# Optimization experiments

Measured on AMD Instinct MI355X. Metric: run time of the kernel, lower is better.

Reference implementation:

```python
import jax, jax.numpy as jnp
import numpy as np

N, E, C = 50000, 600000, 128
BN_EPS = 1e-5
NORM_EPS = 1e-12


def _edgeconv(x, src, dst, wa, ba, g, be, rm, rv, wb, bb):
    # PyG EdgeConv: message = MLP(concat(x_i, x_j - x_i)); aggr='add' at target i
    x_i = x[dst]                      # [E, C] target features
    x_j = x[src]                      # [E, C] source features
    m = jnp.concatenate([x_i, x_j - x_i], axis=-1)   # [E, 2C]
    m = jax.nn.relu(m @ wa.T + ba)                   # Linear(2C->C) + ReLU
    m = (m - rm) * (g * jax.lax.rsqrt(rv + BN_EPS)) + be  # BatchNorm1d (eval)
    m = m @ wb.T + bb                                # Linear(C->C)
    return jax.ops.segment_sum(m, dst, num_segments=x.shape[0])  # [N, C]


def _lin(k, fan_in, shape):
    bound = 1.0 / np.sqrt(fan_in)
    return jax.random.uniform(k, shape, jnp.float32, -bound, bound)


def setup_inputs() -> dict:
    key = jax.random.key(0)
    ks = jax.random.split(key, 16)
    inp = {
        "x": jax.random.normal(ks[0], (N, C), jnp.float32),
        "edge_index": jax.random.randint(ks[1], (2, E), 0, N, jnp.int64),
    }
    # layer 1 params
    inp["w1a"] = _lin(ks[2], 2 * C, (C, 2 * C)); inp["b1a"] = _lin(ks[3], 2 * C, (C,))
    inp["g1"] = jnp.ones((C,), jnp.float32) + 0.1 * jax.random.normal(ks[4], (C,))
    inp["be1"] = 0.1 * jax.random.normal(ks[5], (C,))
    inp["rm1"] = 0.1 * jax.random.normal(ks[6], (C,))
    inp["rv1"] = 0.5 + jax.random.uniform(ks[7], (C,))
    inp["w1b"] = _lin(ks[8], C, (C, C)); inp["b1b"] = _lin(ks[9], C, (C,))
    # layer 2 params
    inp["w2a"] = _lin(ks[10], 2 * C, (C, 2 * C)); inp["b2a"] = _lin(ks[11], 2 * C, (C,))
    inp["g2"] = jnp.ones((C,), jnp.float32) + 0.1 * jax.random.normal(ks[12], (C,))
    inp["be2"] = 0.1 * jax.random.normal(ks[13], (C,))
    inp["rm2"] = 0.1 * jax.random.normal(ks[14], (C,))
    inp["rv2"] = 0.5 + jax.random.uniform(ks[15], (C,))
    k2 = jax.random.split(ks[15], 2)
    inp["w2b"] = _lin(k2[0], C, (C, C)); inp["b2b"] = _lin(k2[1], C, (C,))
    return inp


def reference(x, edge_index, w1a, b1a, g1, be1, rm1, rv1, w1b, b1b,
              w2a, b2a, g2, be2, rm2, rv2, w2b, b2b):
    src, dst = edge_index[0], edge_index[1]
    # layer 1 (all but last): conv -> relu -> L2 normalize -> dropout(eval=identity)
    h = _edgeconv(x, src, dst, w1a, b1a, g1, be1, rm1, rv1, w1b, b1b)
    h = jax.nn.relu(h)
    h = h / jnp.maximum(jnp.linalg.norm(h, axis=-1, keepdims=True), NORM_EPS)
    # last layer: conv only
    return _edgeconv(h, src, dst, w2a, b2a, g2, be2, rm2, rv2, w2b, b2b)
```

## Files before the change

kernel.cpp:

```cpp
#include <hip/hip_runtime.h>

#define CCH 128
#define WPAD 136
typedef unsigned short ushort;
typedef __attribute__((ext_vector_type(8))) short bf16x8_t;
typedef __attribute__((ext_vector_type(4))) float f32x4;

union ABu { bf16x8_t v; ushort u[8]; uint4 q; };

__device__ __forceinline__ ushort f2b(float f) {
  union { float f; unsigned u; } v{f};
  unsigned r = v.u + 0x7fffu + ((v.u >> 16) & 1u);
  return (ushort)(r >> 16);
}
__device__ __forceinline__ float b2f(ushort s) {
  union { unsigned u; float f; } v{(unsigned)s << 16};
  return v.f;
}

__global__ __launch_bounds__(256) void k_pre(const float* __restrict__ w1a,
                                             const float* __restrict__ w1b,
                                             const float* __restrict__ w2a,
                                             const float* __restrict__ w2b,
                                             ushort* __restrict__ Wcat1, ushort* __restrict__ Wb1,
                                             ushort* __restrict__ Wcat2, ushort* __restrict__ Wb2,
                                             const void* __restrict__ ei, int* __restrict__ deg,
                                             int E) {
  const int b = blockIdx.x, t = threadIdx.x;
  if (b < 128) {
    int i = b * 256 + t;
    int c = i >> 7, k = i & 127;
    float v = (c < 128) ? w1a[c * 256 + k] - w1a[c * 256 + 128 + k]
                        : w1a[(c - 128) * 256 + 128 + k];
    Wcat1[i] = f2b(v);
    if (i < 16384) Wb1[i] = f2b(w1b[i]);
  } else if (b < 256) {
    int i = (b - 128) * 256 + t;
    int c = i >> 7, k = i & 127;
    float v = (c < 128) ? w2a[c * 256 + k] - w2a[c * 256 + 128 + k]
                        : w2a[(c - 128) * 256 + 128 + k];
    Wcat2[i] = f2b(v);
    if (i < 16384) Wb2[i] = f2b(w2b[i]);
  } else {
    __shared__ int nz;
    if (t == 0) nz = 0;
    __syncthreads();
    int e = (b - 256) * 256 + t;
    unsigned hi = (e < E) ? ((const unsigned*)ei)[2 * (size_t)e + 1] : 0u;
    if (hi) atomicAdd(&nz, 1);
    __syncthreads();
    bool i64 = (nz == 0);
    if (e < E) {
      int d = i64 ? (int)((const long long*)ei)[(size_t)E + e]
                  : ((const int*)ei)[(size_t)E + e];
      atomicAdd(&deg[d], 1);
    }
  }
}

__global__ __launch_bounds__(256) void k_rowptr(const int* __restrict__ deg,
                                                const int* __restrict__ bsum,
                                                int* __restrict__ rowptr,
                                                int n, int nb, int Etot) {
  __shared__ int s[256];
  const int t = threadIdx.x, b = blockIdx.x;
  s[t] = (t < nb && t < b) ? bsum[t] : 0;
  __syncthreads();
  for (int off = 128; off > 0; off >>= 1) {
    if (t < off) s[t] += s[t + off];
    __syncthreads();
  }
  int boffset = s[0];
  __syncthreads();
  int i = b * 256 + t;
  int v = (i < n) ? deg[i] : 0;
  s[t] = v; __syncthreads();
  for (int off = 1; off < 256; off <<= 1) {
    int tv = (t >= off) ? s[t - off] : 0;
    __syncthreads();
    s[t] += tv;
    __syncthreads();
  }
  if (i < n) rowptr[i] = boffset + s[t] - v;
  if (b == gridDim.x - 1 && t == 0) rowptr[n] = Etot;
}

__global__ __launch_bounds__(256) void k_scatter(const void* __restrict__ ei,
                                                 const int* __restrict__ rowptr,
                                                 int* __restrict__ cnt,
                                                 int* __restrict__ esrc, int E) {
  __shared__ int nz;
  const int t = threadIdx.x;
  if (t == 0) nz = 0;
  __syncthreads();
  int e = blockIdx.x * 256 + t;
  unsigned hi = (e < E) ? ((const unsigned*)ei)[2 * (size_t)e + 1] : 0u;
  if (hi) atomicAdd(&nz, 1);
  __syncthreads();
  bool i64 = (nz == 0);
  if (e < E) {
    int d, sv;
    if (i64) {
      sv = (int)((const long long*)ei)[(size_t)e];
      d  = (int)((const long long*)ei)[(size_t)E + e];
    } else {
      sv = ((const int*)ei)[(size_t)e];
      d  = ((const int*)ei)[(size_t)E + e];
    }
    int pos = rowptr[d] + atomicAdd(&cnt[d], 1);
    esrc[pos] = sv;
  }
}

__device__ __forceinline__ void stage_w(const ushort* __restrict__ Wp,
                                        ushort* __restrict__ wlds, int t) {
  for (int i = t; i < 128 * 16; i += 256) {
    int row = i >> 4, ch = i & 15;
    *(uint4*)&wlds[row * WPAD + ch * 8] = *(const uint4*)&Wp[row * CCH + ch * 8];
  }
}

__device__ __forceinline__ void load_a1_bf16(const ushort* __restrict__ XB,
                                             int ar, int quad, int nN, ABu a[4]) {
#pragma unroll
  for (int kk = 0; kk < 4; ++kk)
    a[kk].q = (ar < nN) ? *(const uint4*)(XB + (size_t)ar * CCH + kk * 32 + quad * 8)
                        : make_uint4(0, 0, 0, 0);
}

__device__ __forceinline__ void load_a1_f32(const float* __restrict__ X,
                                            int ar, int quad, int nN, ABu a[4]) {
#pragma unroll
  for (int kk = 0; kk < 4; ++kk) {
    if (ar < nN) {
      const float* p = X + (size_t)ar * CCH + kk * 32 + quad * 8;
      float4 f0 = *(const float4*)p, f1 = *(const float4*)(p + 4);
      a[kk].u[0] = f2b(f0.x); a[kk].u[1] = f2b(f0.y);
      a[kk].u[2] = f2b(f0.z); a[kk].u[3] = f2b(f0.w);
      a[kk].u[4] = f2b(f1.x); a[kk].u[5] = f2b(f1.y);
      a[kk].u[6] = f2b(f1.z); a[kk].u[7] = f2b(f1.w);
    } else a[kk].q = make_uint4(0, 0, 0, 0);
  }
}

__device__ __forceinline__ void load_a1_lds(const ushort* __restrict__ hlds,
                                            int lr, int quad, ABu a[4]) {
#pragma unroll
  for (int kk = 0; kk < 4; ++kk)
    a[kk].q = *(const uint4*)&hlds[lr * WPAD + kk * 32 + quad * 8];
}

__device__ __forceinline__ void mma1(const ABu a[4],
                                     const ushort* __restrict__ wlds,
                                     int ln, int quad, f32x4 acc[8]) {
#pragma unroll
  for (int s = 0; s < 8; ++s) acc[s] = (f32x4){0.f, 0.f, 0.f, 0.f};
#pragma unroll
  for (int s = 0; s < 8; ++s) {
#pragma unroll
    for (int kk = 0; kk < 4; ++kk) {
      ABu b;
      b.q = *(const uint4*)&wlds[(s * 16 + ln) * WPAD + kk * 32 + quad * 8];
      acc[s] = __builtin_amdgcn_mfma_f32_16x16x32_bf16(a[kk].v, b.v, acc[s], 0, 0, 0);
    }
  }
}

__device__ __forceinline__ void epi1(f32x4 acc[8], int rowb, int ln, int quad, int nN,
                                     const float* bias, int half, ushort* dst) {
#pragma unroll
  for (int s = 0; s < 8; ++s) {
    int col = s * 16 + ln;
    float bv = half ? 0.f : bias[col];
#pragma unroll
    for (int r = 0; r < 4; ++r) {
      int row = rowb + quad * 4 + r;
      if (row < nN) dst[(size_t)row * CCH + col] = f2b(acc[s][r] + bv);
    }
  }
}

__global__ __launch_bounds__(256) void k_mix1(const float* __restrict__ x,
                                              const ushort* __restrict__ Wcat,
                                              const float* __restrict__ bias,
                                              ushort* __restrict__ A1,
                                              ushort* __restrict__ A2, int nN,
                                              const int* __restrict__ deg,
                                              int* __restrict__ bsum, int gG, int n) {
  __shared__ ushort wlds[128 * WPAD];
  const int t = threadIdx.x;
  if ((int)blockIdx.x >= gG) {
    int* s = (int*)wlds;
    int bb = blockIdx.x - gG;
    int i = bb * 256 + t;
    s[t] = (i < n) ? deg[i] : 0;
    __syncthreads();
    for (int off = 128; off > 0; off >>= 1) {
      if (t < off) s[t] += s[t + off];
      __syncthreads();
    }
    if (t == 0) bsum[bb] = s[0];
    return;
  }
  const int wave = t >> 6, lane = t & 63;
  const int ln = lane & 15, quad = lane >> 4;
  const int rowb = blockIdx.x * 64 + wave * 16;
  stage_w(Wcat, wlds, t);
  ABu a[4];
  load_a1_f32(x, rowb + ln, quad, nN, a);
  __syncthreads();
  f32x4 acc[8];
  mma1(a, wlds, ln, quad, acc);
  epi1(acc, rowb, ln, quad, nN, bias, 0, A1);
  __syncthreads();
  stage_w(Wcat + 128 * CCH, wlds, t);
  __syncthreads();
  mma1(a, wlds, ln, quad, acc);
  epi1(acc, rowb, ln, quad, nN, bias, 1, A2);
}

__global__ __launch_bounds__(256) void k_fuse12(const ushort* __restrict__ MB,
                                                const ushort* __restrict__ Wb1,
                                                const float* __restrict__ b1b,
                                                const ushort* __restrict__ Wcat2,
                                                const float* __restrict__ b2a,
                                                const int* __restrict__ deg,
                                                ushort* __restrict__ B0,
                                                ushort* __restrict__ B1, int nN) {
  __shared__ ushort wlds[128 * WPAD];
  __shared__ ushort hlds[64 * WPAD];
  const int t = threadIdx.x, wave = t >> 6, lane = t & 63;
  const int ln = lane & 15, quad = lane >> 4;
  const int rowb = blockIdx.x * 64 + wave * 16;
  const int lrb = wave * 16;

  stage_w(Wb1, wlds, t);
  ABu a[4];
  load_a1_bf16(MB, rowb + ln, quad, nN, a);
  int dg[4];
#pragma unroll
  for (int r = 0; r < 4; ++r) {
    int row = rowb + quad * 4 + r;
    dg[r] = (row < nN) ? deg[row] : 0;
  }
  __syncthreads();
  f32x4 acc[8];
  mma1(a, wlds, ln, quad, acc);

  float biasv[8];
#pragma unroll
  for (int s = 0; s < 8; ++s) biasv[s] = b1b[s * 16 + ln];
#pragma unroll
  for (int r = 0; r < 4; ++r) {
    int row = rowb + quad * 4 + r;
    int lrow = lrb + quad * 4 + r;
    float dn = (float)dg[r];
    float vals[8];
    float ss = 0.f;
#pragma unroll
    for (int s = 0; s < 8; ++s) {
      float v = fmaxf(acc[s][r] + dn * biasv[s], 0.f);
      vals[s] = v;
      ss += v * v;
    }
    ss += __shfl_xor(ss, 1, 64);
    ss += __shfl_xor(ss, 2, 64);
    ss += __shfl_xor(ss, 4, 64);
    ss += __shfl_xor(ss, 8, 64);
    float inv = 1.0f / fmaxf(sqrtf(ss), 1e-12f);
#pragma unroll
    for (int s = 0; s < 8; ++s)
      hlds[lrow * WPAD + s * 16 + ln] = (row < nN) ? f2b(vals[s] * inv) : (ushort)0;
  }
  __syncthreads();

  stage_w(Wcat2, wlds, t);
  load_a1_lds(hlds, lrb + ln, quad, a);
  __syncthreads();
  mma1(a, wlds, ln, quad, acc);
  epi1(acc, rowb, ln, quad, nN, b2a, 0, B0);
  __syncthreads();

  stage_w(Wcat2 + 128 * CCH, wlds, t);
  __syncthreads();
  mma1(a, wlds, ln, quad, acc);
  epi1(acc, rowb, ln, quad, nN, b2a, 1, B1);
}

__global__ __launch_bounds__(256) void k_gemmf(const ushort* __restrict__ XB,
                                               const ushort* __restrict__ W,
                                               const float* __restrict__ bias,
                                               const int* __restrict__ deg,
                                               float* __restrict__ OUT, int nN) {
  __shared__ ushort wlds[128 * WPAD];
  const int t = threadIdx.x;
  stage_w(W, wlds, t);
  const int wave = t >> 6, lane = t & 63;
  const int ln = lane & 15, quad = lane >> 4;
  const int rowb = blockIdx.x * 64 + wave * 16;
  ABu a[4];
  load_a1_bf16(XB, rowb + ln, quad, nN, a);
  int dg[4];
#pragma unroll
  for (int r = 0; r < 4; ++r) {
    int row = rowb + quad * 4 + r;
    dg[r] = (row < nN) ? deg[row] : 0;
  }
  __syncthreads();
  f32x4 acc[8];
  mma1(a, wlds, ln, quad, acc);
  float biasv[8];
#pragma unroll
  for (int s = 0; s < 8; ++s) biasv[s] = bias[s * 16 + ln];
#pragma unroll
  for (int r = 0; r < 4; ++r) {
    int row = rowb + quad * 4 + r;
    if (row >= nN) continue;
    float dn = (float)dg[r];
#pragma unroll
    for (int s = 0; s < 8; ++s)
      OUT[(size_t)row * CCH + s * 16 + ln] = acc[s][r] + dn * biasv[s];
  }
}

__global__ __launch_bounds__(256) void k_aggr(const ushort* __restrict__ A1,
                                              const ushort* __restrict__ A2,
                                              const int* __restrict__ rowptr,
                                              const int* __restrict__ esrc,
                                              const float* __restrict__ g,
                                              const float* __restrict__ be,
                                              const float* __restrict__ rm,
                                              const float* __restrict__ rv,
                                              ushort* __restrict__ M, int nNodes) {
  int node = blockIdx.x * 4 + (threadIdx.x >> 6);
  if (node >= nNodes) return;
  int lane = threadIdx.x & 63;
  int q = lane >> 4;
  int c = (lane & 15) * 8;

  uint4 aq = *(const uint4*)&A1[(size_t)node * CCH + c];
  float a[8] = {b2f((ushort)aq.x), b2f((ushort)(aq.x >> 16)),
                b2f((ushort)aq.y), b2f((ushort)(aq.y >> 16)),
                b2f((ushort)aq.z), b2f((ushort)(aq.z >> 16)),
                b2f((ushort)aq.w), b2f((ushort)(aq.w >> 16))};
  int r0 = rowptr[node], r1 = rowptr[node + 1];
  float s[8] = {0.f, 0.f, 0.f, 0.f, 0.f, 0.f, 0.f, 0.f};

  auto acc8 = [&](uint4 w) {
    const unsigned* p = (const unsigned*)&w;
#pragma unroll
    for (int j = 0; j < 4; ++j) {
      s[2*j]   += fmaxf(a[2*j]   + b2f((ushort)p[j]), 0.f);
      s[2*j+1] += fmaxf(a[2*j+1] + b2f((ushort)(p[j] >> 16)), 0.f);
    }
  };

  for (int base = r0; base < r1; base += 64) {
    int navail = r1 - base; if (navail > 64) navail = 64;
    int myi = (lane < navail) ? esrc[base + lane] : 0;
    int g4 = navail >> 2, tail = navail & 3;
    int j = 0;
    for (; j + 4 <= g4; j += 4) {
      int p0 = j * 4 + q;
      int i0 = __shfl(myi, p0, 64);
      int i1 = __shfl(myi, p0 + 4, 64);
      int i2 = __shfl(myi, p0 + 8, 64);
      int i3 = __shfl(myi, p0 + 12, 64);
      uint4 w0 = *(const uint4*)&A2[(size_t)i0 * CCH + c];
      uint4 w1 = *(const uint4*)&A2[(size_t)i1 * CCH + c];
      uint4 w2 = *(const uint4*)&A2[(size_t)i2 * CCH + c];
      uint4 w3 = *(const uint4*)&A2[(size_t)i3 * CCH + c];
      acc8(w0); acc8(w1); acc8(w2); acc8(w3);
    }
    for (; j < g4; ++j) {
      int i0 = __shfl(myi, j * 4 + q, 64);
      acc8(*(const uint4*)&A2[(size_t)i0 * CCH + c]);
    }
    int pt = g4 * 4 + q; if (pt > 63) pt = 63;
    int it = __shfl(myi, pt, 64);
    if (q < tail) acc8(*(const uint4*)&A2[(size_t)it * CCH + c]);
  }
#pragma unroll
  for (int j = 0; j < 8; ++j) {
    s[j] += __shfl_xor(s[j], 16, 64);
    s[j] += __shfl_xor(s[j], 32, 64);
  }

  if (q == 0) {
    float dn = (float)(r1 - r0);
    unsigned p[4];
#pragma unroll
    for (int j = 0; j < 4; ++j) {
      float sc0 = g[c + 2*j]     * rsqrtf(rv[c + 2*j]     + 1e-5f);
      float sc1 = g[c + 2*j + 1] * rsqrtf(rv[c + 2*j + 1] + 1e-5f);
      float o0 = sc0 * s[2*j]     + dn * (be[c + 2*j]     - rm[c + 2*j]     * sc0);
      float o1 = sc1 * s[2*j + 1] + dn * (be[c + 2*j + 1] - rm[c + 2*j + 1] * sc1);
      p[j] = (unsigned)f2b(o0) | ((unsigned)f2b(o1) << 16);
    }
    *(uint4*)&M[(size_t)node * CCH + c] = make_uint4(p[0], p[1], p[2], p[3]);
  }
}

extern "C" void kernel_launch(void* const* d_in, const int* in_sizes, int n_in,
                              void* d_out, int out_size, void* d_ws, size_t ws_size,
                              hipStream_t stream) {
  const float* x   = (const float*)d_in[0];
  const void*  ei  = d_in[1];
  const float* w1a = (const float*)d_in[2];
  const float* b1a = (const float*)d_in[3];
  const float* g1  = (const float*)d_in[4];
  const float* be1 = (const float*)d_in[5];
  const float* rm1 = (const float*)d_in[6];
  const float* rv1 = (const float*)d_in[7];
  const float* w1b = (const float*)d_in[8];
  const float* b1b = (const float*)d_in[9];
  const float* w2a = (const float*)d_in[10];
  const float* b2a = (const float*)d_in[11];
  const float* g2  = (const float*)d_in[12];
  const float* be2 = (const float*)d_in[13];
  const float* rm2 = (const float*)d_in[14];
  const float* rv2 = (const float*)d_in[15];
  const float* w2b = (const float*)d_in[16];
  const float* b2b = (const float*)d_in[17];

  const int N = in_sizes[0] / CCH;
  const int E = in_sizes[1] / 2;
  const size_t NC = (size_t)N * CCH;

  int* deg    = (int*)d_ws;
  int* cnt    = deg + N;
  int* rowptr = cnt + N;
  int* bsum   = rowptr + N + 1;
  int* esrc   = bsum + 256;
  uintptr_t pw = ((uintptr_t)(esrc + E) + 63) & ~(uintptr_t)63;
  ushort* Wcat1 = (ushort*)pw;
  ushort* Wcat2 = Wcat1 + 32768;
  ushort* Wb1   = Wcat2 + 32768;
  ushort* Wb2   = Wb1 + 16384;
  uintptr_t pb = ((uintptr_t)(Wb2 + 16384) + 63) & ~(uintptr_t)63;
  ushort* B0 = (ushort*)pb;
  ushort* B1 = B0 + NC;
  ushort* MB = B1 + NC;

  const int gE  = (E + 255) / 256;
  const int gS  = (N + 255) / 256;
  const int gG  = (N + 63) / 64;
  const int gA  = (N + 3) / 4;

  hipMemsetAsync(deg, 0, sizeof(int) * 2 * (size_t)N, stream);
  k_pre<<<256 + gE, 256, 0, stream>>>(w1a, w1b, w2a, w2b,
                                      Wcat1, Wb1, Wcat2, Wb2, ei, deg, E);
  k_mix1<<<gG + gS, 256, 0, stream>>>(x, Wcat1, b1a, B0, B1, N, deg, bsum, gG, N);
  k_rowptr<<<gS, 256, 0, stream>>>(deg, bsum, rowptr, N, gS, E);
  k_scatter<<<gE, 256, 0, stream>>>(ei, rowptr, cnt, esrc, E);

  k_aggr<<<gA, 256, 0, stream>>>(B0, B1, rowptr, esrc, g1, be1, rm1, rv1, MB, N);
  k_fuse12<<<gG, 256, 0, stream>>>(MB, Wb1, b1b, Wcat2, b2a, deg, B0, B1, N);
  k_aggr<<<gA, 256, 0, stream>>>(B0, B1, rowptr, esrc, g2, be2, rm2, rv2, MB, N);
  k_gemmf<<<gG, 256, 0, stream>>>(MB, Wb2, b2b, deg, (float*)d_out, N);
}
```

Before: 299.2 us.

## Make node GEMM kernels persistent with weights staged once in LDS

The three node-level GEMM kernels (k_mix1, k_fuse12, k_gemmf) become persistent grids of 256 blocks with 512 threads. Each block stages all its weight matrices into LDS once, then loops over 128-row tiles, so the per-block weight reload and intermediate barriers go away. The aggregation gather loop is also restructured into fixed batches of four clamped loads with predicated accumulation, which drops the separate tail paths. The cost is much larger LDS use per block (up to about 135KB in k_fuse12), which lowers occupancy.

```diff
diff --git a/kernel.cpp b/kernel.cpp
--- a/kernel.cpp
+++ b/kernel.cpp
@@ -112,14 +112,6 @@
   }
 }
 
-__device__ __forceinline__ void stage_w(const ushort* __restrict__ Wp,
-                                        ushort* __restrict__ wlds, int t) {
-  for (int i = t; i < 128 * 16; i += 256) {
-    int row = i >> 4, ch = i & 15;
-    *(uint4*)&wlds[row * WPAD + ch * 8] = *(const uint4*)&Wp[row * CCH + ch * 8];
-  }
-}
-
 __device__ __forceinline__ void load_a1_bf16(const ushort* __restrict__ XB,
                                              int ar, int quad, int nN, ABu a[4]) {
 #pragma unroll
@@ -180,20 +172,20 @@
   }
 }
 
-__global__ __launch_bounds__(256) void k_mix1(const float* __restrict__ x,
+__global__ __launch_bounds__(512) void k_mix1(const float* __restrict__ x,
                                               const ushort* __restrict__ Wcat,
                                               const float* __restrict__ bias,
                                               ushort* __restrict__ A1,
                                               ushort* __restrict__ A2, int nN,
                                               const int* __restrict__ deg,
-                                              int* __restrict__ bsum, int gG, int n) {
-  __shared__ ushort wlds[128 * WPAD];
+                                              int* __restrict__ bsum, int gG, int nT, int n) {
+  __shared__ ushort wlds[2 * 128 * WPAD];
   const int t = threadIdx.x;
   if ((int)blockIdx.x >= gG) {
     int* s = (int*)wlds;
     int bb = blockIdx.x - gG;
     int i = bb * 256 + t;
-    s[t] = (i < n) ? deg[i] : 0;
+    if (t < 256) s[t] = (i < n) ? deg[i] : 0;
     __syncthreads();
     for (int off = 128; off > 0; off >>= 1) {
       if (t < off) s[t] += s[t + off];
@@ -202,124 +194,134 @@
     if (t == 0) bsum[bb] = s[0];
     return;
   }
+  for (int i = t; i < 2 * 128 * 16; i += 512) {
+    int h = i >> 11, j = i & 2047;
+    int row = j >> 4, ch = j & 15;
+    *(uint4*)&wlds[(h * 128 + row) * WPAD + ch * 8] =
+        *(const uint4*)&Wcat[(size_t)h * 128 * CCH + row * CCH + ch * 8];
+  }
+  __syncthreads();
   const int wave = t >> 6, lane = t & 63;
   const int ln = lane & 15, quad = lane >> 4;
-  const int rowb = blockIdx.x * 64 + wave * 16;
-  stage_w(Wcat, wlds, t);
-  ABu a[4];
-  load_a1_f32(x, rowb + ln, quad, nN, a);
-  __syncthreads();
-  f32x4 acc[8];
-  mma1(a, wlds, ln, quad, acc);
-  epi1(acc, rowb, ln, quad, nN, bias, 0, A1);
-  __syncthreads();
-  stage_w(Wcat + 128 * CCH, wlds, t);
-  __syncthreads();
-  mma1(a, wlds, ln, quad, acc);
-  epi1(acc, rowb, ln, quad, nN, bias, 1, A2);
-}
-
-__global__ __launch_bounds__(256) void k_fuse12(const ushort* __restrict__ MB,
+  for (int tile = blockIdx.x; tile < nT; tile += gG) {
+    const int rowb = tile * 128 + wave * 16;
+    ABu a[4];
+    load_a1_f32(x, rowb + ln, quad, nN, a);
+    f32x4 acc[8];
+    mma1(a, wlds, ln, quad, acc);
+    epi1(acc, rowb, ln, quad, nN, bias, 0, A1);
+    mma1(a, wlds + 128 * WPAD, ln, quad, acc);
+    epi1(acc, rowb, ln, quad, nN, bias, 1, A2);
+  }
+}
+
+__global__ __launch_bounds__(512) void k_fuse12(const ushort* __restrict__ MB,
                                                 const ushort* __restrict__ Wb1,
                                                 const float* __restrict__ b1b,
                                                 const ushort* __restrict__ Wcat2,
                                                 const float* __restrict__ b2a,
                                                 const int* __restrict__ deg,
                                                 ushort* __restrict__ B0,
-                                                ushort* __restrict__ B1, int nN) {
-  __shared__ ushort wlds[128 * WPAD];
-  __shared__ ushort hlds[64 * WPAD];
-  const int t = threadIdx.x, wave = t >> 6, lane = t & 63;
+                                                ushort* __restrict__ B1, int nN,
+                                                int nT, int gG) {
+  __shared__ ushort wlds[3 * 128 * WPAD];
+  __shared__ ushort hlds[8 * 16 * WPAD];
+  const int t = threadIdx.x;
+  for (int i = t; i < 3 * 128 * 16; i += 512) {
+    int h = i >> 11, j = i & 2047;
+    int row = j >> 4, ch = j & 15;
+    const ushort* src = (h == 0) ? &Wb1[row * CCH + ch * 8]
+                                 : &Wcat2[(size_t)(h - 1) * 128 * CCH + row * CCH + ch * 8];
+    *(uint4*)&wlds[(h * 128 + row) * WPAD + ch * 8] = *(const uint4*)src;
+  }
+  __syncthreads();
+  const int wave = t >> 6, lane = t & 63;
   const int ln = lane & 15, quad = lane >> 4;
-  const int rowb = blockIdx.x * 64 + wave * 16;
-  const int lrb = wave * 16;
-
-  stage_w(Wb1, wlds, t);
-  ABu a[4];
-  load_a1_bf16(MB, rowb + ln, quad, nN, a);
-  int dg[4];
-#pragma unroll
-  for (int r = 0; r < 4; ++r) {
-    int row = rowb + quad * 4 + r;
-    dg[r] = (row < nN) ? deg[row] : 0;
-  }
-  __syncthreads();
-  f32x4 acc[8];
-  mma1(a, wlds, ln, quad, acc);
-
+  ushort* hw = &hlds[wave * 16 * WPAD];
   float biasv[8];
 #pragma unroll
   for (int s = 0; s < 8; ++s) biasv[s] = b1b[s * 16 + ln];
-#pragma unroll
-  for (int r = 0; r < 4; ++r) {
-    int row = rowb + quad * 4 + r;
-    int lrow = lrb + quad * 4 + r;
-    float dn = (float)dg[r];
-    float vals[8];
-    float ss = 0.f;
-#pragma unroll
-    for (int s = 0; s < 8; ++s) {
-      float v = fmaxf(acc[s][r] + dn * biasv[s], 0.f);
-      vals[s] = v;
-      ss += v * v;
-    }
-    ss += __shfl_xor(ss, 1, 64);
-    ss += __shfl_xor(ss, 2, 64);
-    ss += __shfl_xor(ss, 4, 64);
-    ss += __shfl_xor(ss, 8, 64);
-    float inv = 1.0f / fmaxf(sqrtf(ss), 1e-12f);
-#pragma unroll
-    for (int s = 0; s < 8; ++s)
-      hlds[lrow * WPAD + s * 16 + ln] = (row < nN) ? f2b(vals[s] * inv) : (ushort)0;
-  }
-  __syncthreads();
-
-  stage_w(Wcat2, wlds, t);
-  load_a1_lds(hlds, lrb + ln, quad, a);
-  __syncthreads();
-  mma1(a, wlds, ln, quad, acc);
-  epi1(acc, rowb, ln, quad, nN, b2a, 0, B0);
-  __syncthreads();
-
-  stage_w(Wcat2 + 128 * CCH, wlds, t);
-  __syncthreads();
-  mma1(a, wlds, ln, quad, acc);
-  epi1(acc, rowb, ln, quad, nN, b2a, 1, B1);
-}
-
-__global__ __launch_bounds__(256) void k_gemmf(const ushort* __restrict__ XB,
+  for (int tile = blockIdx.x; tile < nT; tile += gG) {
+    const int rowb = tile * 128 + wave * 16;
+    ABu a[4];
+    load_a1_bf16(MB, rowb + ln, quad, nN, a);
+    int dg[4];
+#pragma unroll
+    for (int r = 0; r < 4; ++r) {
+      int row = rowb + quad * 4 + r;
+      dg[r] = (row < nN) ? deg[row] : 0;
+    }
+    f32x4 acc[8];
+    mma1(a, wlds, ln, quad, acc);
+#pragma unroll
+    for (int r = 0; r < 4; ++r) {
+      int row = rowb + quad * 4 + r;
+      int lrow = quad * 4 + r;
+      float dn = (float)dg[r];
+      float vals[8];
+      float ss = 0.f;
+#pragma unroll
+      for (int s = 0; s < 8; ++s) {
+        float v = fmaxf(acc[s][r] + dn * biasv[s], 0.f);
+        vals[s] = v;
+        ss += v * v;
+      }
+      ss += __shfl_xor(ss, 1, 64);
+      ss += __shfl_xor(ss, 2, 64);
+      ss += __shfl_xor(ss, 4, 64);
+      ss += __shfl_xor(ss, 8, 64);
+      float inv = 1.0f / fmaxf(sqrtf(ss), 1e-12f);
+#pragma unroll
+      for (int s = 0; s < 8; ++s)
+        hw[lrow * WPAD + s * 16 + ln] = (row < nN) ? f2b(vals[s] * inv) : (ushort)0;
+    }
+    load_a1_lds(hw, ln, quad, a);
+    mma1(a, wlds + 128 * WPAD, ln, quad, acc);
+    epi1(acc, rowb, ln, quad, nN, b2a, 0, B0);
+    mma1(a, wlds + 2 * 128 * WPAD, ln, quad, acc);
+    epi1(acc, rowb, ln, quad, nN, b2a, 1, B1);
+  }
+}
+
+__global__ __launch_bounds__(512) void k_gemmf(const ushort* __restrict__ XB,
                                                const ushort* __restrict__ W,
                                                const float* __restrict__ bias,
                                                const int* __restrict__ deg,
-                                               float* __restrict__ OUT, int nN) {
+                                               float* __restrict__ OUT, int nN,
+                                               int nT, int gG) {
   __shared__ ushort wlds[128 * WPAD];
   const int t = threadIdx.x;
-  stage_w(W, wlds, t);
+  for (int i = t; i < 128 * 16; i += 512) {
+    int row = i >> 4, ch = i & 15;
+    *(uint4*)&wlds[row * WPAD + ch * 8] = *(const uint4*)&W[row * CCH + ch * 8];
+  }
+  __syncthreads();
   const int wave = t >> 6, lane = t & 63;
   const int ln = lane & 15, quad = lane >> 4;
-  const int rowb = blockIdx.x * 64 + wave * 16;
-  ABu a[4];
-  load_a1_bf16(XB, rowb + ln, quad, nN, a);
-  int dg[4];
-#pragma unroll
-  for (int r = 0; r < 4; ++r) {
-    int row = rowb + quad * 4 + r;
-    dg[r] = (row < nN) ? deg[row] : 0;
-  }
-  __syncthreads();
-  f32x4 acc[8];
-  mma1(a, wlds, ln, quad, acc);
   float biasv[8];
 #pragma unroll
   for (int s = 0; s < 8; ++s) biasv[s] = bias[s * 16 + ln];
-#pragma unroll
-  for (int r = 0; r < 4; ++r) {
-    int row = rowb + quad * 4 + r;
-    if (row >= nN) continue;
-    float dn = (float)dg[r];
-#pragma unroll
-    for (int s = 0; s < 8; ++s)
-      OUT[(size_t)row * CCH + s * 16 + ln] = acc[s][r] + dn * biasv[s];
+  for (int tile = blockIdx.x; tile < nT; tile += gG) {
+    const int rowb = tile * 128 + wave * 16;
+    ABu a[4];
+    load_a1_bf16(XB, rowb + ln, quad, nN, a);
+    int dg[4];
+#pragma unroll
+    for (int r = 0; r < 4; ++r) {
+      int row = rowb + quad * 4 + r;
+      dg[r] = (row < nN) ? deg[row] : 0;
+    }
+    f32x4 acc[8];
+    mma1(a, wlds, ln, quad, acc);
+#pragma unroll
+    for (int r = 0; r < 4; ++r) {
+      int row = rowb + quad * 4 + r;
+      if (row >= nN) continue;
+      float dn = (float)dg[r];
+#pragma unroll
+      for (int s = 0; s < 8; ++s)
+        OUT[(size_t)row * CCH + s * 16 + ln] = acc[s][r] + dn * biasv[s];
+    }
   }
 }
 
@@ -358,27 +360,22 @@
   for (int base = r0; base < r1; base += 64) {
     int navail = r1 - base; if (navail > 64) navail = 64;
     int myi = (lane < navail) ? esrc[base + lane] : 0;
-    int g4 = navail >> 2, tail = navail & 3;
-    int j = 0;
-    for (; j + 4 <= g4; j += 4) {
-      int p0 = j * 4 + q;
-      int i0 = __shfl(myi, p0, 64);
-      int i1 = __shfl(myi, p0 + 4, 64);
-      int i2 = __shfl(myi, p0 + 8, 64);
-      int i3 = __shfl(myi, p0 + 12, 64);
-      uint4 w0 = *(const uint4*)&A2[(size_t)i0 * CCH + c];
-      uint4 w1 = *(const uint4*)&A2[(size_t)i1 * CCH + c];
-      uint4 w2 = *(const uint4*)&A2[(size_t)i2 * CCH + c];
-      uint4 w3 = *(const uint4*)&A2[(size_t)i3 * CCH + c];
-      acc8(w0); acc8(w1); acc8(w2); acc8(w3);
-    }
-    for (; j < g4; ++j) {
-      int i0 = __shfl(myi, j * 4 + q, 64);
-      acc8(*(const uint4*)&A2[(size_t)i0 * CCH + c]);
-    }
-    int pt = g4 * 4 + q; if (pt > 63) pt = 63;
-    int it = __shfl(myi, pt, 64);
-    if (q < tail) acc8(*(const uint4*)&A2[(size_t)it * CCH + c]);
+    int nr = (navail + 3) >> 2;
+    for (int j0 = 0; j0 < nr; j0 += 4) {
+      uint4 w[4];
+      int pe[4];
+#pragma unroll
+      for (int u = 0; u < 4; ++u) {
+        int p = (j0 + u) * 4 + q;
+        pe[u] = p;
+        int pc = (p < navail) ? p : (navail - 1);
+        int idx = __shfl(myi, pc, 64);
+        w[u] = *(const uint4*)&A2[(size_t)idx * CCH + c];
+      }
+#pragma unroll
+      for (int u = 0; u < 4; ++u)
+        if (pe[u] < navail) acc8(w[u]);
+    }
   }
 #pragma unroll
   for (int j = 0; j < 8; ++j) {
@@ -442,20 +439,21 @@
   ushort* B1 = B0 + NC;
   ushort* MB = B1 + NC;
 
-  const int gE  = (E + 255) / 256;
-  const int gS  = (N + 255) / 256;
-  const int gG  = (N + 63) / 64;
-  const int gA  = (N + 3) / 4;
+  const int gE = (E + 255) / 256;
+  const int gS = (N + 255) / 256;
+  const int gP = 256;
+  const int nT = (N + 127) / 128;
+  const int gA = (N + 3) / 4;
 
   hipMemsetAsync(deg, 0, sizeof(int) * 2 * (size_t)N, stream);
   k_pre<<<256 + gE, 256, 0, stream>>>(w1a, w1b, w2a, w2b,
                                       Wcat1, Wb1, Wcat2, Wb2, ei, deg, E);
-  k_mix1<<<gG + gS, 256, 0, stream>>>(x, Wcat1, b1a, B0, B1, N, deg, bsum, gG, N);
+  k_mix1<<<gP + gS, 512, 0, stream>>>(x, Wcat1, b1a, B0, B1, N, deg, bsum, gP, nT, N);
   k_rowptr<<<gS, 256, 0, stream>>>(deg, bsum, rowptr, N, gS, E);
   k_scatter<<<gE, 256, 0, stream>>>(ei, rowptr, cnt, esrc, E);
 
   k_aggr<<<gA, 256, 0, stream>>>(B0, B1, rowptr, esrc, g1, be1, rm1, rv1, MB, N);
-  k_fuse12<<<gG, 256, 0, stream>>>(MB, Wb1, b1b, Wcat2, b2a, deg, B0, B1, N);
+  k_fuse12<<<gP, 512, 0, stream>>>(MB, Wb1, b1b, Wcat2, b2a, deg, B0, B1, N, nT, gP);
   k_aggr<<<gA, 256, 0, stream>>>(B0, B1, rowptr, esrc, g2, be2, rm2, rv2, MB, N);
-  k_gemmf<<<gG, 256, 0, stream>>>(MB, Wb2, b2b, deg, (float*)d_out, N);
-}
+  k_gemmf<<<gP, 512, 0, stream>>>(MB, Wb2, b2b, deg, (float*)d_out, N, nT, gP);
+}
```

Result: slower. 341.0 us (+14.0%).

## Fuse weight prep, layer-1 GEMM and degree count into one kernel

Applied to the files above, without the earlier changes.

Merges the weight-conversion, degree-count and first-layer mixing kernels into one launch. Each GEMM block now builds the bf16 difference weights from fp32 w1a directly in LDS, which removes one launch and the Wcat1 round trip but repeats the conversion in every block. k_rowptr now computes block offsets by having each block re-sum all preceding degrees instead of reading precomputed block sums, which is quadratic total work. The aggregation gather loop is rewritten to issue four loads up front with clamped indices and predicated accumulation, simplifying the tail handling.

```diff
diff --git a/kernel.cpp b/kernel.cpp
--- a/kernel.cpp
+++ b/kernel.cpp
@@ -18,34 +18,132 @@
   return v.f;
 }
 
-__global__ __launch_bounds__(256) void k_pre(const float* __restrict__ w1a,
-                                             const float* __restrict__ w1b,
-                                             const float* __restrict__ w2a,
-                                             const float* __restrict__ w2b,
-                                             ushort* __restrict__ Wcat1, ushort* __restrict__ Wb1,
-                                             ushort* __restrict__ Wcat2, ushort* __restrict__ Wb2,
-                                             const void* __restrict__ ei, int* __restrict__ deg,
-                                             int E) {
+__device__ __forceinline__ void stage_w(const ushort* __restrict__ Wp,
+                                        ushort* __restrict__ wlds, int t) {
+  for (int i = t; i < 128 * 16; i += 256) {
+    int row = i >> 4, ch = i & 15;
+    *(uint4*)&wlds[row * WPAD + ch * 8] = *(const uint4*)&Wp[row * CCH + ch * 8];
+  }
+}
+
+__device__ __forceinline__ void load_a1_bf16(const ushort* __restrict__ XB,
+                                             int ar, int quad, int nN, ABu a[4]) {
+#pragma unroll
+  for (int kk = 0; kk < 4; ++kk)
+    a[kk].q = (ar < nN) ? *(const uint4*)(XB + (size_t)ar * CCH + kk * 32 + quad * 8)
+                        : make_uint4(0, 0, 0, 0);
+}
+
+__device__ __forceinline__ void load_a1_f32(const float* __restrict__ X,
+                                            int ar, int quad, int nN, ABu a[4]) {
+#pragma unroll
+  for (int kk = 0; kk < 4; ++kk) {
+    if (ar < nN) {
+      const float* p = X + (size_t)ar * CCH + kk * 32 + quad * 8;
+      float4 f0 = *(const float4*)p, f1 = *(const float4*)(p + 4);
+      a[kk].u[0] = f2b(f0.x); a[kk].u[1] = f2b(f0.y);
+      a[kk].u[2] = f2b(f0.z); a[kk].u[3] = f2b(f0.w);
+      a[kk].u[4] = f2b(f1.x); a[kk].u[5] = f2b(f1.y);
+      a[kk].u[6] = f2b(f1.z); a[kk].u[7] = f2b(f1.w);
+    } else a[kk].q = make_uint4(0, 0, 0, 0);
+  }
+}
+
+__device__ __forceinline__ void load_a1_lds(const ushort* __restrict__ hlds,
+                                            int lr, int quad, ABu a[4]) {
+#pragma unroll
+  for (int kk = 0; kk < 4; ++kk)
+    a[kk].q = *(const uint4*)&hlds[lr * WPAD + kk * 32 + quad * 8];
+}
+
+__device__ __forceinline__ void mma1(const ABu a[4],
+                                     const ushort* __restrict__ wlds,
+                                     int ln, int quad, f32x4 acc[8]) {
+#pragma unroll
+  for (int s = 0; s < 8; ++s) acc[s] = (f32x4){0.f, 0.f, 0.f, 0.f};
+#pragma unroll
+  for (int s = 0; s < 8; ++s) {
+#pragma unroll
+    for (int kk = 0; kk < 4; ++kk) {
+      ABu b;
+      b.q = *(const uint4*)&wlds[(s * 16 + ln) * WPAD + kk * 32 + quad * 8];
+      acc[s] = __builtin_amdgcn_mfma_f32_16x16x32_bf16(a[kk].v, b.v, acc[s], 0, 0, 0);
+    }
+  }
+}
+
+__device__ __forceinline__ void epi1(f32x4 acc[8], int rowb, int ln, int quad, int nN,
+                                     const float* bias, int half, ushort* dst) {
+#pragma unroll
+  for (int s = 0; s < 8; ++s) {
+    int col = s * 16 + ln;
+    float bv = half ? 0.f : bias[col];
+#pragma unroll
+    for (int r = 0; r < 4; ++r) {
+      int row = rowb + quad * 4 + r;
+      if (row < nN) dst[(size_t)row * CCH + col] = f2b(acc[s][r] + bv);
+    }
+  }
+}
+
+__global__ __launch_bounds__(256) void k_mega1(const float* __restrict__ x,
+                                               const float* __restrict__ w1a,
+                                               const float* __restrict__ bias,
+                                               ushort* __restrict__ A1,
+                                               ushort* __restrict__ A2, int nN,
+                                               const float* __restrict__ w2a,
+                                               const float* __restrict__ w1b,
+                                               const float* __restrict__ w2b,
+                                               ushort* __restrict__ Wcat2,
+                                               ushort* __restrict__ Wb1,
+                                               ushort* __restrict__ Wb2,
+                                               const void* __restrict__ ei,
+                                               int* __restrict__ deg, int E, int gB) {
+  __shared__ ushort wlds[128 * WPAD];
   const int b = blockIdx.x, t = threadIdx.x;
-  if (b < 128) {
-    int i = b * 256 + t;
-    int c = i >> 7, k = i & 127;
-    float v = (c < 128) ? w1a[c * 256 + k] - w1a[c * 256 + 128 + k]
-                        : w1a[(c - 128) * 256 + 128 + k];
-    Wcat1[i] = f2b(v);
-    if (i < 16384) Wb1[i] = f2b(w1b[i]);
-  } else if (b < 256) {
-    int i = (b - 128) * 256 + t;
+  if (b < gB) {
+    const int wave = t >> 6, lane = t & 63;
+    const int ln = lane & 15, quad = lane >> 4;
+    const int rowb = b * 64 + wave * 16;
+    for (int i = t; i < 2048; i += 256) {
+      int c = i >> 4, k8 = (i & 15) * 8;
+      const float* p = w1a + c * 256 + k8;
+      float4 l0 = *(const float4*)p, l1 = *(const float4*)(p + 4);
+      float4 r0 = *(const float4*)(p + 128), r1 = *(const float4*)(p + 132);
+      ushort o[8] = {f2b(l0.x - r0.x), f2b(l0.y - r0.y), f2b(l0.z - r0.z), f2b(l0.w - r0.w),
+                     f2b(l1.x - r1.x), f2b(l1.y - r1.y), f2b(l1.z - r1.z), f2b(l1.w - r1.w)};
+      *(uint4*)&wlds[c * WPAD + k8] = *(const uint4*)o;
+    }
+    ABu a[4];
+    load_a1_f32(x, rowb + ln, quad, nN, a);
+    __syncthreads();
+    f32x4 acc[8];
+    mma1(a, wlds, ln, quad, acc);
+    epi1(acc, rowb, ln, quad, nN, bias, 0, A1);
+    __syncthreads();
+    for (int i = t; i < 2048; i += 256) {
+      int c = i >> 4, k8 = (i & 15) * 8;
+      const float* p = w1a + c * 256 + 128 + k8;
+      float4 r0 = *(const float4*)p, r1 = *(const float4*)(p + 4);
+      ushort o[8] = {f2b(r0.x), f2b(r0.y), f2b(r0.z), f2b(r0.w),
+                     f2b(r1.x), f2b(r1.y), f2b(r1.z), f2b(r1.w)};
+      *(uint4*)&wlds[c * WPAD + k8] = *(const uint4*)o;
+    }
+    __syncthreads();
+    mma1(a, wlds, ln, quad, acc);
+    epi1(acc, rowb, ln, quad, nN, bias, 1, A2);
+  } else if (b < gB + 128) {
+    int i = (b - gB) * 256 + t;
     int c = i >> 7, k = i & 127;
     float v = (c < 128) ? w2a[c * 256 + k] - w2a[c * 256 + 128 + k]
                         : w2a[(c - 128) * 256 + 128 + k];
     Wcat2[i] = f2b(v);
-    if (i < 16384) Wb2[i] = f2b(w2b[i]);
+    if (i < 16384) { Wb1[i] = f2b(w1b[i]); Wb2[i] = f2b(w2b[i]); }
   } else {
     __shared__ int nz;
     if (t == 0) nz = 0;
     __syncthreads();
-    int e = (b - 256) * 256 + t;
+    int e = (b - gB - 128) * 256 + t;
     unsigned hi = (e < E) ? ((const unsigned*)ei)[2 * (size_t)e + 1] : 0u;
     if (hi) atomicAdd(&nz, 1);
     __syncthreads();
@@ -59,12 +157,14 @@
 }
 
 __global__ __launch_bounds__(256) void k_rowptr(const int* __restrict__ deg,
-                                                const int* __restrict__ bsum,
                                                 int* __restrict__ rowptr,
-                                                int n, int nb, int Etot) {
+                                                int n, int Etot) {
   __shared__ int s[256];
   const int t = threadIdx.x, b = blockIdx.x;
-  s[t] = (t < nb && t < b) ? bsum[t] : 0;
+  int lim = b * 256;
+  int partial = 0;
+  for (int i = t; i < lim; i += 256) partial += deg[i];
+  s[t] = partial;
   __syncthreads();
   for (int off = 128; off > 0; off >>= 1) {
     if (t < off) s[t] += s[t + off];
@@ -110,113 +210,6 @@
     int pos = rowptr[d] + atomicAdd(&cnt[d], 1);
     esrc[pos] = sv;
   }
-}
-
-__device__ __forceinline__ void stage_w(const ushort* __restrict__ Wp,
-                                        ushort* __restrict__ wlds, int t) {
-  for (int i = t; i < 128 * 16; i += 256) {
-    int row = i >> 4, ch = i & 15;
-    *(uint4*)&wlds[row * WPAD + ch * 8] = *(const uint4*)&Wp[row * CCH + ch * 8];
-  }
-}
-
-__device__ __forceinline__ void load_a1_bf16(const ushort* __restrict__ XB,
-                                             int ar, int quad, int nN, ABu a[4]) {
-#pragma unroll
-  for (int kk = 0; kk < 4; ++kk)
-    a[kk].q = (ar < nN) ? *(const uint4*)(XB + (size_t)ar * CCH + kk * 32 + quad * 8)
-                        : make_uint4(0, 0, 0, 0);
-}
-
-__device__ __forceinline__ void load_a1_f32(const float* __restrict__ X,
-                                            int ar, int quad, int nN, ABu a[4]) {
-#pragma unroll
-  for (int kk = 0; kk < 4; ++kk) {
-    if (ar < nN) {
-      const float* p = X + (size_t)ar * CCH + kk * 32 + quad * 8;
-      float4 f0 = *(const float4*)p, f1 = *(const float4*)(p + 4);
-      a[kk].u[0] = f2b(f0.x); a[kk].u[1] = f2b(f0.y);
-      a[kk].u[2] = f2b(f0.z); a[kk].u[3] = f2b(f0.w);
-      a[kk].u[4] = f2b(f1.x); a[kk].u[5] = f2b(f1.y);
-      a[kk].u[6] = f2b(f1.z); a[kk].u[7] = f2b(f1.w);
-    } else a[kk].q = make_uint4(0, 0, 0, 0);
-  }
-}
-
-__device__ __forceinline__ void load_a1_lds(const ushort* __restrict__ hlds,
-                                            int lr, int quad, ABu a[4]) {
-#pragma unroll
-  for (int kk = 0; kk < 4; ++kk)
-    a[kk].q = *(const uint4*)&hlds[lr * WPAD + kk * 32 + quad * 8];
-}
-
-__device__ __forceinline__ void mma1(const ABu a[4],
-                                     const ushort* __restrict__ wlds,
-                                     int ln, int quad, f32x4 acc[8]) {
-#pragma unroll
-  for (int s = 0; s < 8; ++s) acc[s] = (f32x4){0.f, 0.f, 0.f, 0.f};
-#pragma unroll
-  for (int s = 0; s < 8; ++s) {
-#pragma unroll
-    for (int kk = 0; kk < 4; ++kk) {
-      ABu b;
-      b.q = *(const uint4*)&wlds[(s * 16 + ln) * WPAD + kk * 32 + quad * 8];
-      acc[s] = __builtin_amdgcn_mfma_f32_16x16x32_bf16(a[kk].v, b.v, acc[s], 0, 0, 0);
-    }
-  }
-}
-
-__device__ __forceinline__ void epi1(f32x4 acc[8], int rowb, int ln, int quad, int nN,
-                                     const float* bias, int half, ushort* dst) {
-#pragma unroll
-  for (int s = 0; s < 8; ++s) {
-    int col = s * 16 + ln;
-    float bv = half ? 0.f : bias[col];
-#pragma unroll
-    for (int r = 0; r < 4; ++r) {
-      int row = rowb + quad * 4 + r;
-      if (row < nN) dst[(size_t)row * CCH + col] = f2b(acc[s][r] + bv);
-    }
-  }
-}
-
-__global__ __launch_bounds__(256) void k_mix1(const float* __restrict__ x,
-                                              const ushort* __restrict__ Wcat,
-                                              const float* __restrict__ bias,
-                                              ushort* __restrict__ A1,
-                                              ushort* __restrict__ A2, int nN,
-                                              const int* __restrict__ deg,
-                                              int* __restrict__ bsum, int gG, int n) {
-  __shared__ ushort wlds[128 * WPAD];
-  const int t = threadIdx.x;
-  if ((int)blockIdx.x >= gG) {
-    int* s = (int*)wlds;
-    int bb = blockIdx.x - gG;
-    int i = bb * 256 + t;
-    s[t] = (i < n) ? deg[i] : 0;
-    __syncthreads();
-    for (int off = 128; off > 0; off >>= 1) {
-      if (t < off) s[t] += s[t + off];
-      __syncthreads();
-    }
-    if (t == 0) bsum[bb] = s[0];
-    return;
-  }
-  const int wave = t >> 6, lane = t & 63;
-  const int ln = lane & 15, quad = lane >> 4;
-  const int rowb = blockIdx.x * 64 + wave * 16;
-  stage_w(Wcat, wlds, t);
-  ABu a[4];
-  load_a1_f32(x, rowb + ln, quad, nN, a);
-  __syncthreads();
-  f32x4 acc[8];
-  mma1(a, wlds, ln, quad, acc);
-  epi1(acc, rowb, ln, quad, nN, bias, 0, A1);
-  __syncthreads();
-  stage_w(Wcat + 128 * CCH, wlds, t);
-  __syncthreads();
-  mma1(a, wlds, ln, quad, acc);
-  epi1(acc, rowb, ln, quad, nN, bias, 1, A2);
 }
 
 __global__ __launch_bounds__(256) void k_fuse12(const ushort* __restrict__ MB,
@@ -358,27 +351,22 @@
   for (int base = r0; base < r1; base += 64) {
     int navail = r1 - base; if (navail > 64) navail = 64;
     int myi = (lane < navail) ? esrc[base + lane] : 0;
-    int g4 = navail >> 2, tail = navail & 3;
-    int j = 0;
-    for (; j + 4 <= g4; j += 4) {
-      int p0 = j * 4 + q;
-      int i0 = __shfl(myi, p0, 64);
-      int i1 = __shfl(myi, p0 + 4, 64);
-      int i2 = __shfl(myi, p0 + 8, 64);
-      int i3 = __shfl(myi, p0 + 12, 64);
-      uint4 w0 = *(const uint4*)&A2[(size_t)i0 * CCH + c];
-      uint4 w1 = *(const uint4*)&A2[(size_t)i1 * CCH + c];
-      uint4 w2 = *(const uint4*)&A2[(size_t)i2 * CCH + c];
-      uint4 w3 = *(const uint4*)&A2[(size_t)i3 * CCH + c];
-      acc8(w0); acc8(w1); acc8(w2); acc8(w3);
-    }
-    for (; j < g4; ++j) {
-      int i0 = __shfl(myi, j * 4 + q, 64);
-      acc8(*(const uint4*)&A2[(size_t)i0 * CCH + c]);
-    }
-    int pt = g4 * 4 + q; if (pt > 63) pt = 63;
-    int it = __shfl(myi, pt, 64);
-    if (q < tail) acc8(*(const uint4*)&A2[(size_t)it * CCH + c]);
+    int nr = (navail + 3) >> 2;
+    for (int j0 = 0; j0 < nr; j0 += 4) {
+      uint4 w[4];
+      int pe[4];
+#pragma unroll
+      for (int u = 0; u < 4; ++u) {
+        int p = (j0 + u) * 4 + q;
+        pe[u] = p;
+        int pc = (p < navail) ? p : (navail - 1);
+        int idx = __shfl(myi, pc, 64);
+        w[u] = *(const uint4*)&A2[(size_t)idx * CCH + c];
+      }
+#pragma unroll
+      for (int u = 0; u < 4; ++u)
+        if (pe[u] < navail) acc8(w[u]);
+    }
   }
 #pragma unroll
   for (int j = 0; j < 8; ++j) {
@@ -430,11 +418,9 @@
   int* deg    = (int*)d_ws;
   int* cnt    = deg + N;
   int* rowptr = cnt + N;
-  int* bsum   = rowptr + N + 1;
-  int* esrc   = bsum + 256;
+  int* esrc   = rowptr + N + 1;
   uintptr_t pw = ((uintptr_t)(esrc + E) + 63) & ~(uintptr_t)63;
-  ushort* Wcat1 = (ushort*)pw;
-  ushort* Wcat2 = Wcat1 + 32768;
+  ushort* Wcat2 = (ushort*)pw;
   ushort* Wb1   = Wcat2 + 32768;
   ushort* Wb2   = Wb1 + 16384;
   uintptr_t pb = ((uintptr_t)(Wb2 + 16384) + 63) & ~(uintptr_t)63;
@@ -444,18 +430,18 @@
 
   const int gE  = (E + 255) / 256;
   const int gS  = (N + 255) / 256;
-  const int gG  = (N + 63) / 64;
+  const int gG2 = (N + 63) / 64;
   const int gA  = (N + 3) / 4;
 
   hipMemsetAsync(deg, 0, sizeof(int) * 2 * (size_t)N, stream);
-  k_pre<<<256 + gE, 256, 0, stream>>>(w1a, w1b, w2a, w2b,
-                                      Wcat1, Wb1, Wcat2, Wb2, ei, deg, E);
-  k_mix1<<<gG + gS, 256, 0, stream>>>(x, Wcat1, b1a, B0, B1, N, deg, bsum, gG, N);
-  k_rowptr<<<gS, 256, 0, stream>>>(deg, bsum, rowptr, N, gS, E);
+  k_mega1<<<gG2 + 128 + gE, 256, 0, stream>>>(x, w1a, b1a, B0, B1, N,
+                                              w2a, w1b, w2b, Wcat2, Wb1, Wb2,
+                                              ei, deg, E, gG2);
+  k_rowptr<<<gS, 256, 0, stream>>>(deg, rowptr, N, E);
   k_scatter<<<gE, 256, 0, stream>>>(ei, rowptr, cnt, esrc, E);
 
   k_aggr<<<gA, 256, 0, stream>>>(B0, B1, rowptr, esrc, g1, be1, rm1, rv1, MB, N);
-  k_fuse12<<<gG, 256, 0, stream>>>(MB, Wb1, b1b, Wcat2, b2a, deg, B0, B1, N);
+  k_fuse12<<<gG2, 256, 0, stream>>>(MB, Wb1, b1b, Wcat2, b2a, deg, B0, B1, N);
   k_aggr<<<gA, 256, 0, stream>>>(B0, B1, rowptr, esrc, g2, be2, rm2, rv2, MB, N);
-  k_gemmf<<<gG, 256, 0, stream>>>(MB, Wb2, b2b, deg, (float*)d_out, N);
-}
+  k_gemmf<<<gG2, 256, 0, stream>>>(MB, Wb2, b2b, deg, (float*)d_out, N);
+}
```

Measured after the change: 308.7 us. 3.2% more time.
